# Kernel optimization log

Hardware: AMD Instinct MI355X
Metric: run time of the kernel (lower is better)

Reference implementation:

```python
import jax, jax.numpy as jnp
import numpy as np

# Dimensions
B, T_ENC, T_DEC = 64, 128, 64          # batch, encoder frames, max_video_length
DH, DV, CHUNK = 1024, 2048, 8          # dim_hidden, dim_video, ON-LSTM chunk size
NCH = DV // CHUNK                      # number of chunks (256)
G = 4 * DV + 2 * NCH                   # gate width of ON-LSTM cell


def setup_inputs() -> dict:
    key = jax.random.key(0)
    ks = jax.random.split(key, 6)
    s = lambda n: 1.0 / np.sqrt(n)
    return {
        "encoder_outputs": jax.random.normal(ks[0], (B, T_ENC, DH), jnp.float32),
        "encoder_hidden": jnp.zeros((1, B, DH), jnp.float32),  # unused by forward
        # Attention_update params: score over concat(enc_feat, query)
        "W_att1": (jax.random.normal(ks[1], (DH + DV, DH), jnp.float32) * s(DH + DV)),
        "b_att1": jnp.zeros((DH,), jnp.float32),
        "w_att2": (jax.random.normal(ks[2], (DH,), jnp.float32) * s(DH)),
        # ON-LSTM cell params (single layer: input DH -> hidden DV)
        "W_ih": (jax.random.normal(ks[3], (DH, G), jnp.float32) * s(DH)),
        "b_ih": jnp.zeros((G,), jnp.float32),
        "W_hh": (jax.random.normal(ks[4], (DV, G), jnp.float32) * s(DV)),
        "b_hh": jnp.zeros((G,), jnp.float32),
    }


def cumsoftmax(x):
    return jnp.cumsum(jax.nn.softmax(x, axis=-1), axis=-1)


def _decode(encoder_outputs, W_att1, b_att1, w_att2, W_ih, b_ih, W_hh, b_hh):
    b = encoder_outputs.shape[0]
    t_enc = encoder_outputs.shape[1]
    h0 = jnp.zeros((b, DV), encoder_outputs.dtype)
    c0 = jnp.zeros((b, NCH, CHUNK), encoder_outputs.dtype)

    def step(carry, _):
        h, c = carry
        # --- attention: additive score over encoder outputs, query = hidden ---
        q = jnp.broadcast_to(h[:, None, :], (b, t_enc, DV))
        feat = jnp.concatenate([encoder_outputs, q], axis=-1)        # (B,T,DH+DV)
        e = jnp.tanh(feat @ W_att1 + b_att1) @ w_att2                # (B,T)
        alpha = jax.nn.softmax(e, axis=-1)
        context = jnp.einsum("bt,btd->bd", alpha, encoder_outputs)  # (B,DH)
        # --- ON-LSTM cell ---
        gates = context @ W_ih + b_ih + h @ W_hh + b_hh              # (B,G)
        cingate = 1.0 - cumsoftmax(gates[:, :NCH])                   # master input gate
        cforgetgate = cumsoftmax(gates[:, NCH:2 * NCH])              # master forget gate
        r = gates[:, 2 * NCH:].reshape(b, 4 * NCH, CHUNK)
        o = jax.nn.sigmoid(r[:, :NCH])
        g = jnp.tanh(r[:, NCH:2 * NCH])
        i = jax.nn.sigmoid(r[:, 2 * NCH:3 * NCH])
        f = jax.nn.sigmoid(r[:, 3 * NCH:])
        cin = cingate[:, :, None]
        cfg = cforgetgate[:, :, None]
        overlap = cfg * cin
        fgate = f * overlap + (cfg - overlap)
        igate = i * overlap + (cin - overlap)
        cy = fgate * c + igate * g                                   # (B,NCH,CHUNK)
        hy = (o * jnp.tanh(cy)).reshape(b, DV)
        return (hy, cy), hy

    (_, _), outs = jax.lax.scan(step, (h0, c0), None, length=T_DEC)
    return jnp.transpose(outs, (1, 0, 2))  # (B, T_DEC, DV)


def reference(encoder_outputs, encoder_hidden, W_att1, b_att1, w_att2, W_ih, b_ih, W_hh, b_hh):
    return _decode(encoder_outputs, W_att1, b_att1, w_att2, W_ih, b_ih, W_hh, b_hh)
```

## Files before the change

kernel.cpp:

```cpp
#include <hip/hip_runtime.h>
#include <math.h>

#define BB   64
#define TENC 128
#define TDEC 64
#define DHH  1024
#define DVV  2048
#define NCHN 256
#define GG   8704
#define KTOT 3072

typedef unsigned short u16;
typedef __bf16 bf16x8 __attribute__((ext_vector_type(8)));
typedef float  f32x4  __attribute__((ext_vector_type(4)));

__device__ __forceinline__ float sigmoidf_(float x) { return 1.f / (1.f + expf(-x)); }
__device__ __forceinline__ u16 f2bf(float f) {
    unsigned u = __float_as_uint(f);
    unsigned r = (u + 0x7fffu + ((u >> 16) & 1u)) >> 16;
    return (u16)r;
}
__device__ __forceinline__ float bf2f(u16 s) { return __uint_as_float(((unsigned)s) << 16); }


__global__ __launch_bounds__(256) void k_P(const float* __restrict__ enc,
                                           const float* __restrict__ W1,
                                           const float* __restrict__ b1,
                                           float* __restrict__ P) {
    __shared__ float As[32][68];
    __shared__ float Bs[32][68];
    int j0 = blockIdx.x * 64;
    int m0 = blockIdx.y * 64;
    int tid = threadIdx.x;
    int jg = tid & 15, bg = tid >> 4;
    float acc[4][4] = {};
    for (int k0 = 0; k0 < DHH; k0 += 32) {
#pragma unroll
        for (int p = 0; p < 8; ++p) {
            int r = p * 8 + (tid >> 5);
            int kk = tid & 31;
            As[kk][r] = enc[(size_t)(m0 + r) * DHH + k0 + kk];
        }
#pragma unroll
        for (int p = 0; p < 8; ++p) {
            int kk = p * 4 + (tid >> 6);
            int jl = tid & 63;
            Bs[kk][jl] = W1[(size_t)(k0 + kk) * DHH + j0 + jl];
        }
        __syncthreads();
#pragma unroll
        for (int kk = 0; kk < 32; ++kk) {
            float4 a = *(const float4*)&As[kk][bg * 4];
            float4 b = *(const float4*)&Bs[kk][jg * 4];
            float av[4] = {a.x, a.y, a.z, a.w};
            float bv[4] = {b.x, b.y, b.z, b.w};
#pragma unroll
            for (int i = 0; i < 4; ++i)
#pragma unroll
                for (int j = 0; j < 4; ++j) acc[i][j] += av[i] * bv[j];
        }
        __syncthreads();
    }
    float4 bb = *(const float4*)&b1[j0 + jg * 4];
    float bia[4] = {bb.x, bb.y, bb.z, bb.w};
#pragma unroll
    for (int i = 0; i < 4; ++i) {
        int r = m0 + bg * 4 + i;
        float4 v = make_float4(acc[i][0] + bia[0], acc[i][1] + bia[1],
                               acc[i][2] + bia[2], acc[i][3] + bia[3]);
        *(float4*)&P[(size_t)r * DHH + j0 + jg * 4] = v;
    }
}

__global__ __launch_bounds__(256) void k_e(const float* __restrict__ P,
                                           const float* __restrict__ hWp,
                                           const float* __restrict__ w2,
                                           float* __restrict__ e) {
    int b = blockIdx.x, tg = blockIdx.y;
    __shared__ float hw[DHH];
    __shared__ float w2s[DHH];
    int tid = threadIdx.x;
#pragma unroll
    for (int p = 0; p < 4; ++p) {
        int d = p * 256 + tid;
        float s = 0.f;
#pragma unroll
        for (int ks = 0; ks < 8; ++ks) s += hWp[(ks * 64 + b) * DHH + d];
        hw[d] = s;
        w2s[d] = w2[d];
    }
    __syncthreads();
    int wave = tid >> 6, lane = tid & 63;
    const float* Pb = P + (size_t)b * TENC * DHH;
    for (int tt = 0; tt < 8; ++tt) {
        int t = tg * 32 + wave * 8 + tt;
        const float* Pr = Pb + (size_t)t * DHH;
        float s = 0.f;
#pragma unroll
        for (int i = 0; i < 16; ++i) {
            int d = i * 64 + lane;
            s += tanhf(Pr[d] + hw[d]) * w2s[d];
        }
#pragma unroll
        for (int off = 32; off > 0; off >>= 1) s += __shfl_down(s, off);
        if (lane == 0) e[b * TENC + t] = s;
    }
}


__global__ __launch_bounds__(256) void k_init2(float* __restrict__ c,
                                               u16* __restrict__ xh,
                                               u16* __restrict__ xl) {
    int i = blockIdx.x * 256 + threadIdx.x;
    xh[i] = 0; xl[i] = 0;
    if (i < BB * DVV) c[i] = 0.f;
}

template <bool LO>
__global__ __launch_bounds__(256) void k_cvt(const float* __restrict__ S1,
                                             const float* __restrict__ S2,
                                             int K1, int N, int K,
                                             u16* __restrict__ Dh,
                                             u16* __restrict__ Dl) {
    __shared__ float t[64][65];
    int n0 = blockIdx.x * 64, k0 = blockIdx.y * 64;
    int tid = threadIdx.x;
    int cn = tid & 63, r4 = tid >> 6;
#pragma unroll
    for (int p = 0; p < 16; ++p) {
        int kk = p * 4 + r4;
        int kg = k0 + kk;
        const float* src = (kg < K1) ? S1 + (size_t)kg * N : S2 + (size_t)(kg - K1) * N;
        t[kk][cn] = src[n0 + cn];
    }
    __syncthreads();
    int ck = tid & 63, n4 = tid >> 6;
#pragma unroll
    for (int p = 0; p < 16; ++p) {
        int nn = p * 4 + n4;
        float w = t[ck][nn];
        u16 hi = f2bf(w);
        size_t o = (size_t)(n0 + nn) * K + k0 + ck;
        Dh[o] = hi;
        if (LO) Dl[o] = f2bf(w - bf2f(hi));
    }
}

__global__ __launch_bounds__(256) void k_mma1(const u16* __restrict__ xh,
                                              const u16* __restrict__ Wta,
                                              float* __restrict__ hWp) {
    int n0 = blockIdx.x * 64;
    int kseg = blockIdx.y;
    int wv = threadIdx.x >> 6, l = threadIdx.x & 63;
    int lr = l & 15, lk = (l >> 4) * 8;
    int n = n0 + wv * 16 + lr;
    const u16* wp = Wta + (size_t)n * 2048 + lk;
    const u16* ap = xh + (size_t)lr * KTOT + 1024 + lk;
    f32x4 z = {0.f, 0.f, 0.f, 0.f};
    f32x4 acc[4];
#pragma unroll
    for (int mf = 0; mf < 4; ++mf) acc[mf] = z;
    int kend = kseg * 256 + 256;
    for (int k = kseg * 256; k < kend; k += 32) {
        bf16x8 bfrag = *(const bf16x8*)(wp + k);
#pragma unroll
        for (int mf = 0; mf < 4; ++mf) {
            bf16x8 a = *(const bf16x8*)(ap + (size_t)mf * 16 * KTOT + k);
            acc[mf] = __builtin_amdgcn_mfma_f32_16x16x32_bf16(a, bfrag, acc[mf], 0, 0, 0);
        }
    }
    float* dst = hWp + (size_t)kseg * 64 * DHH;
#pragma unroll
    for (int mf = 0; mf < 4; ++mf)
#pragma unroll
        for (int r = 0; r < 4; ++r) {
            int m = mf * 16 + (l >> 4) * 4 + r;
            dst[(size_t)m * DHH + n] = acc[mf][r];
        }
}

__global__ __launch_bounds__(256) void k_mma3(const u16* __restrict__ xh,
                                              const u16* __restrict__ xl,
                                              const u16* __restrict__ Wh,
                                              const u16* __restrict__ Wl,
                                              float* __restrict__ part) {
    int n0 = blockIdx.x * 64;
    int kseg = blockIdx.y;
    int wv = threadIdx.x >> 6, l = threadIdx.x & 63;
    int lr = l & 15, lk = (l >> 4) * 8;
    int n = n0 + wv * 16 + lr;
    const u16* wph = Wh + (size_t)n * KTOT + lk;
    const u16* wpl = Wl + (size_t)n * KTOT + lk;
    const u16* aph = xh + (size_t)lr * KTOT + lk;
    const u16* apl = xl + (size_t)lr * KTOT + lk;
    f32x4 z = {0.f, 0.f, 0.f, 0.f};
    f32x4 acc[4];
#pragma unroll
    for (int mf = 0; mf < 4; ++mf) acc[mf] = z;
    int kend = kseg * 1536 + 1536;
    for (int k = kseg * 1536; k < kend; k += 32) {
        bf16x8 bh = *(const bf16x8*)(wph + k);
        bf16x8 bl = *(const bf16x8*)(wpl + k);
#pragma unroll
        for (int mf = 0; mf < 4; ++mf) {
            size_t ao = (size_t)mf * 16 * KTOT + k;
            bf16x8 ah = *(const bf16x8*)(aph + ao);
            bf16x8 al = *(const bf16x8*)(apl + ao);
            acc[mf] = __builtin_amdgcn_mfma_f32_16x16x32_bf16(ah, bh, acc[mf], 0, 0, 0);
            acc[mf] = __builtin_amdgcn_mfma_f32_16x16x32_bf16(ah, bl, acc[mf], 0, 0, 0);
            acc[mf] = __builtin_amdgcn_mfma_f32_16x16x32_bf16(al, bh, acc[mf], 0, 0, 0);
        }
    }
    float* dst = part + (size_t)kseg * 64 * GG;
#pragma unroll
    for (int mf = 0; mf < 4; ++mf)
#pragma unroll
        for (int r = 0; r < 4; ++r) {
            int m = mf * 16 + (l >> 4) * 4 + r;
            dst[(size_t)m * GG + n] = acc[mf][r];
        }
}

__global__ __launch_bounds__(256) void k_sc2(const float* __restrict__ e,
                                             const float* __restrict__ enc,
                                             u16* __restrict__ xh,
                                             u16* __restrict__ xl) {
    int b = blockIdx.x, dg = blockIdx.y;
    __shared__ float al[TENC];
    __shared__ float red[256];
    int tid = threadIdx.x;
    float v = (tid < TENC) ? e[b * TENC + tid] : -3.0e38f;
    red[tid] = v;
    __syncthreads();
    for (int s = 128; s > 0; s >>= 1) {
        if (tid < s) red[tid] = fmaxf(red[tid], red[tid + s]);
        __syncthreads();
    }
    float mx = red[0];
    __syncthreads();
    float ex = (tid < TENC) ? expf(v - mx) : 0.f;
    red[tid] = ex;
    __syncthreads();
    for (int s = 128; s > 0; s >>= 1) {
        if (tid < s) red[tid] += red[tid + s];
        __syncthreads();
    }
    float inv = 1.f / red[0];
    if (tid < TENC) al[tid] = ex * inv;
    __syncthreads();
    int d = dg * 256 + tid;
    const float* ep = enc + (size_t)b * TENC * DHH + d;
    float acc = 0.f;
#pragma unroll 4
    for (int t = 0; t < TENC; ++t) acc += al[t] * ep[(size_t)t * DHH];
    u16 hi = f2bf(acc);
    xh[(size_t)b * KTOT + d] = hi;
    xl[(size_t)b * KTOT + d] = f2bf(acc - bf2f(hi));
}

__global__ __launch_bounds__(256) void k_pw2(const float* __restrict__ part,
                                             const float* __restrict__ bih,
                                             const float* __restrict__ bhh,
                                             u16* __restrict__ xh,
                                             u16* __restrict__ xl,
                                             float* __restrict__ c,
                                             float* __restrict__ out, int t) {
    int b = blockIdx.x;
    __shared__ float g[GG];
    __shared__ float cs1[NCHN], cs2[NCHN], t1[NCHN], t2[NCHN];
    int tid = threadIdx.x;
    for (int p = 0; p < 34; ++p) {
        int j = p * 256 + tid;
        float s = bih[j] + bhh[j] + part[(size_t)b * GG + j] + part[(size_t)(64 + b) * GG + j];
        g[j] = s;
    }
    __syncthreads();
    float x1 = g[tid], x2 = g[NCHN + tid];
    t1[tid] = x1; t2[tid] = x2;
    __syncthreads();
    for (int s = 128; s > 0; s >>= 1) {
        if (tid < s) { t1[tid] = fmaxf(t1[tid], t1[tid + s]); t2[tid] = fmaxf(t2[tid], t2[tid + s]); }
        __syncthreads();
    }
    float m1 = t1[0], m2 = t2[0];
    __syncthreads();
    float e1 = expf(x1 - m1), e2 = expf(x2 - m2);
    t1[tid] = e1; t2[tid] = e2;
    __syncthreads();
    for (int s = 128; s > 0; s >>= 1) {
        if (tid < s) { t1[tid] += t1[tid + s]; t2[tid] += t2[tid + s]; }
        __syncthreads();
    }
    float inv1 = 1.f / t1[0], inv2 = 1.f / t2[0];
    __syncthreads();
    cs1[tid] = e1; cs2[tid] = e2;
    __syncthreads();
    for (int off = 1; off < NCHN; off <<= 1) {
        float a1 = (tid >= off) ? cs1[tid - off] : 0.f;
        float a2 = (tid >= off) ? cs2[tid - off] : 0.f;
        __syncthreads();
        cs1[tid] += a1; cs2[tid] += a2;
        __syncthreads();
    }
    float* cb = c + (size_t)b * DVV;
    float* ob = out + ((size_t)b * TDEC + t) * DVV;
    u16* xhb = xh + (size_t)b * KTOT + 1024;
    u16* xlb = xl + (size_t)b * KTOT + 1024;
    for (int p = 0; p < 8; ++p) {
        int idx = p * 256 + tid;
        int ch = idx >> 3;
        float cin = 1.f - cs1[ch] * inv1;
        float cfg = cs2[ch] * inv2;
        float ov = cfg * cin;
        float oo = sigmoidf_(g[512 + idx]);
        float gg = tanhf(g[2560 + idx]);
        float ii = sigmoidf_(g[4608 + idx]);
        float ff = sigmoidf_(g[6656 + idx]);
        float fg = ff * ov + (cfg - ov);
        float ig = ii * ov + (cin - ov);
        float cy = fg * cb[idx] + ig * gg;
        cb[idx] = cy;
        float hy = oo * tanhf(cy);
        ob[idx] = hy;
        u16 hh = f2bf(hy);
        xhb[idx] = hh;
        xlb[idx] = f2bf(hy - bf2f(hh));
    }
}


__global__ __launch_bounds__(256) void k_init(float* __restrict__ h, float* __restrict__ c) {
    int i = blockIdx.x * 256 + threadIdx.x;
    h[i] = 0.f;
    c[i] = 0.f;
}

template <int KS>
__global__ __launch_bounds__(256) void k_skinny(const float* __restrict__ A1,
                                                const float* __restrict__ A2,
                                                const float* __restrict__ B1,
                                                const float* __restrict__ B2,
                                                int K1, int K2, int N,
                                                float* __restrict__ part) {
    __shared__ float As[32][68];
    __shared__ float Bs[32][68];
    int j0 = blockIdx.x * 64;
    int kseg = blockIdx.y;
    int tid = threadIdx.x;
    int jg = tid & 15, bg = tid >> 4;
    float acc[4][4] = {};
    for (int k0 = kseg * KS; k0 < (kseg + 1) * KS; k0 += 32) {
#pragma unroll
        for (int p = 0; p < 8; ++p) {
            int r = p * 8 + (tid >> 5);
            int kk = tid & 31;
            int k = k0 + kk;
            As[kk][r] = (k < K1) ? A1[r * K1 + k] : A2[r * K2 + (k - K1)];
        }
#pragma unroll
        for (int p = 0; p < 8; ++p) {
            int kk = p * 4 + (tid >> 6);
            int jl = tid & 63;
            int k = k0 + kk;
            Bs[kk][jl] = (k < K1) ? B1[(size_t)k * N + j0 + jl]
                                  : B2[(size_t)(k - K1) * N + j0 + jl];
        }
        __syncthreads();
#pragma unroll
        for (int kk = 0; kk < 32; ++kk) {
            float4 a = *(const float4*)&As[kk][bg * 4];
            float4 b = *(const float4*)&Bs[kk][jg * 4];
            float av[4] = {a.x, a.y, a.z, a.w};
            float bv[4] = {b.x, b.y, b.z, b.w};
#pragma unroll
            for (int i = 0; i < 4; ++i)
#pragma unroll
                for (int j = 0; j < 4; ++j) acc[i][j] += av[i] * bv[j];
        }
        __syncthreads();
    }
#pragma unroll
    for (int i = 0; i < 4; ++i) {
        int r = bg * 4 + i;
        float4 v = make_float4(acc[i][0], acc[i][1], acc[i][2], acc[i][3]);
        *(float4*)&part[(size_t)(kseg * 64 + r) * N + j0 + jg * 4] = v;
    }
}

__global__ __launch_bounds__(256) void k_sc_f32(const float* __restrict__ e,
                                                const float* __restrict__ enc,
                                                float* __restrict__ ctx) {
    int b = blockIdx.x, dg = blockIdx.y;
    __shared__ float al[TENC];
    __shared__ float red[256];
    int tid = threadIdx.x;
    float v = (tid < TENC) ? e[b * TENC + tid] : -3.0e38f;
    red[tid] = v;
    __syncthreads();
    for (int s = 128; s > 0; s >>= 1) {
        if (tid < s) red[tid] = fmaxf(red[tid], red[tid + s]);
        __syncthreads();
    }
    float mx = red[0];
    __syncthreads();
    float ex = (tid < TENC) ? expf(v - mx) : 0.f;
    red[tid] = ex;
    __syncthreads();
    for (int s = 128; s > 0; s >>= 1) {
        if (tid < s) red[tid] += red[tid + s];
        __syncthreads();
    }
    float inv = 1.f / red[0];
    if (tid < TENC) al[tid] = ex * inv;
    __syncthreads();
    int d = dg * 256 + tid;
    const float* ep = enc + (size_t)b * TENC * DHH + d;
    float acc = 0.f;
#pragma unroll 4
    for (int t = 0; t < TENC; ++t) acc += al[t] * ep[(size_t)t * DHH];
    ctx[b * DHH + d] = acc;
}

__global__ __launch_bounds__(256) void k_pw_f32(const float* __restrict__ part,
                                                const float* __restrict__ bih,
                                                const float* __restrict__ bhh,
                                                float* __restrict__ h,
                                                float* __restrict__ c,
                                                float* __restrict__ out, int t) {
    int b = blockIdx.x;
    __shared__ float g[GG];
    __shared__ float cs1[NCHN], cs2[NCHN], t1[NCHN], t2[NCHN];
    int tid = threadIdx.x;
    for (int p = 0; p < 34; ++p) {
        int j = p * 256 + tid;
        float s = bih[j] + bhh[j];
#pragma unroll
        for (int ks = 0; ks < 6; ++ks) s += part[(size_t)(ks * 64 + b) * GG + j];
        g[j] = s;
    }
    __syncthreads();
    float x1 = g[tid], x2 = g[NCHN + tid];
    t1[tid] = x1; t2[tid] = x2;
    __syncthreads();
    for (int s = 128; s > 0; s >>= 1) {
        if (tid < s) { t1[tid] = fmaxf(t1[tid], t1[tid + s]); t2[tid] = fmaxf(t2[tid], t2[tid + s]); }
        __syncthreads();
    }
    float m1 = t1[0], m2 = t2[0];
    __syncthreads();
    float e1 = expf(x1 - m1), e2 = expf(x2 - m2);
    t1[tid] = e1; t2[tid] = e2;
    __syncthreads();
    for (int s = 128; s > 0; s >>= 1) {
        if (tid < s) { t1[tid] += t1[tid + s]; t2[tid] += t2[tid + s]; }
        __syncthreads();
    }
    float inv1 = 1.f / t1[0], inv2 = 1.f / t2[0];
    __syncthreads();
    cs1[tid] = e1; cs2[tid] = e2;
    __syncthreads();
    for (int off = 1; off < NCHN; off <<= 1) {
        float a1 = (tid >= off) ? cs1[tid - off] : 0.f;
        float a2 = (tid >= off) ? cs2[tid - off] : 0.f;
        __syncthreads();
        cs1[tid] += a1; cs2[tid] += a2;
        __syncthreads();
    }
    float* cb = c + (size_t)b * DVV;
    float* hb = h + (size_t)b * DVV;
    float* ob = out + ((size_t)b * TDEC + t) * DVV;
    for (int p = 0; p < 8; ++p) {
        int idx = p * 256 + tid;
        int ch = idx >> 3;
        float cin = 1.f - cs1[ch] * inv1;
        float cfg = cs2[ch] * inv2;
        float ov = cfg * cin;
        float oo = sigmoidf_(g[512 + idx]);
        float gg = tanhf(g[2560 + idx]);
        float ii = sigmoidf_(g[4608 + idx]);
        float ff = sigmoidf_(g[6656 + idx]);
        float fg = ff * ov + (cfg - ov);
        float ig = ii * ov + (cin - ov);
        float cy = fg * cb[idx] + ig * gg;
        cb[idx] = cy;
        float hy = oo * tanhf(cy);
        hb[idx] = hy;
        ob[idx] = hy;
    }
}


extern "C" void kernel_launch(void* const* d_in, const int* in_sizes, int n_in,
                              void* d_out, int out_size, void* d_ws, size_t ws_size,
                              hipStream_t stream) {
    const float* enc    = (const float*)d_in[0];
    const float* W_att1 = (const float*)d_in[2];
    const float* b_att1 = (const float*)d_in[3];
    const float* w_att2 = (const float*)d_in[4];
    const float* W_ih   = (const float*)d_in[5];
    const float* b_ih   = (const float*)d_in[6];
    const float* W_hh   = (const float*)d_in[7];
    const float* b_hh   = (const float*)d_in[8];
    float* out = (float*)d_out;
    float* ws  = (float*)d_ws;

    if (ws_size >= 152600576ull) {
        float* P    = ws;
        float* hWp  = P + 8388608;
        float* ebuf = hWp + 524288;
        float* gp   = ebuf + 8192;
        float* c    = gp + 1114112;
        u16* xh  = (u16*)(c + 131072);
        u16* xl  = xh + 196608;
        u16* Wth = xl + 196608;
        u16* Wtl = Wth + 26738688;
        u16* Wta = Wtl + 26738688;

        k_init2<<<768, 256, 0, stream>>>(c, xh, xl);
        k_cvt<true><<<dim3(136, 48), 256, 0, stream>>>(W_ih, W_hh, 1024, GG, KTOT, Wth, Wtl);
        const float* Wh_att = W_att1 + 1024 * 1024;
        k_cvt<false><<<dim3(16, 32), 256, 0, stream>>>(Wh_att, Wh_att, 2048, DHH, 2048, Wta, Wta);
        k_P<<<dim3(16, 128), 256, 0, stream>>>(enc, W_att1, b_att1, P);

        for (int t = 0; t < TDEC; ++t) {
            k_mma1<<<dim3(16, 8), 256, 0, stream>>>(xh, Wta, hWp);
            k_e<<<dim3(BB, 4), 256, 0, stream>>>(P, hWp, w_att2, ebuf);
            k_sc2<<<dim3(BB, 4), 256, 0, stream>>>(ebuf, enc, xh, xl);
            k_mma3<<<dim3(136, 2), 256, 0, stream>>>(xh, xl, Wth, Wtl, gp);
            k_pw2<<<BB, 256, 0, stream>>>(gp, b_ih, b_hh, xh, xl, c, out, t);
        }
    } else if (ws_size >= 12591104ull * 4ull) {
        float* P    = ws;
        float* hWp  = P + 8388608;
        float* ebuf = hWp + 524288;
        float* ctx  = ebuf + 8192;
        float* gp   = ctx + 65536;
        float* h    = gp + 3342336;
        float* c    = h + 131072;

        k_init<<<512, 256, 0, stream>>>(h, c);
        k_P<<<dim3(16, 128), 256, 0, stream>>>(enc, W_att1, b_att1, P);

        const float* Wh_att = W_att1 + 1024 * 1024;
        for (int t = 0; t < TDEC; ++t) {
            k_skinny<256><<<dim3(16, 8), 256, 0, stream>>>(h, h, Wh_att, Wh_att,
                                                           2048, 2048, DHH, hWp);
            k_e<<<dim3(BB, 4), 256, 0, stream>>>(P, hWp, w_att2, ebuf);
            k_sc_f32<<<dim3(BB, 4), 256, 0, stream>>>(ebuf, enc, ctx);
            k_skinny<512><<<dim3(136, 6), 256, 0, stream>>>(ctx, h, W_ih, W_hh,
                                                            1024, 2048, GG, gp);
            k_pw_f32<<<BB, 256, 0, stream>>>(gp, b_ih, b_hh, h, c, out, t);
        }
    }
}
```

Measured before the change: 12.10 ms.

## Move precompute GEMM to split-bf16 MFMA, add in-block K-split and fast math

```diff
diff --git a/kernel.cpp b/kernel.cpp
--- a/kernel.cpp
+++ b/kernel.cpp
@@ -14,14 +14,110 @@
 typedef __bf16 bf16x8 __attribute__((ext_vector_type(8)));
 typedef float  f32x4  __attribute__((ext_vector_type(4)));
 
-__device__ __forceinline__ float sigmoidf_(float x) { return 1.f / (1.f + expf(-x)); }
 __device__ __forceinline__ u16 f2bf(float f) {
     unsigned u = __float_as_uint(f);
     unsigned r = (u + 0x7fffu + ((u >> 16) & 1u)) >> 16;
     return (u16)r;
 }
 __device__ __forceinline__ float bf2f(u16 s) { return __uint_as_float(((unsigned)s) << 16); }
-
+__device__ __forceinline__ float tanh_fast(float x) {
+    float xc = fminf(fmaxf(x, -15.f), 15.f);
+    float t = __expf(2.f * xc);
+    return 1.f - 2.f * __builtin_amdgcn_rcpf(t + 1.f);
+}
+__device__ __forceinline__ float sigmoid_fast(float x) {
+    float xc = fminf(fmaxf(x, -30.f), 30.f);
+    return __builtin_amdgcn_rcpf(1.f + __expf(-xc));
+}
+
+
+__global__ __launch_bounds__(256) void k_init2(float* __restrict__ c,
+                                               u16* __restrict__ xh,
+                                               u16* __restrict__ xl) {
+    int i = blockIdx.x * 256 + threadIdx.x;
+    xh[i] = 0; xl[i] = 0;
+    if (i < BB * DVV) c[i] = 0.f;
+}
+
+template <bool LO>
+__global__ __launch_bounds__(256) void k_cvt(const float* __restrict__ S1,
+                                             const float* __restrict__ S2,
+                                             int K1, int N, int K,
+                                             u16* __restrict__ Dh,
+                                             u16* __restrict__ Dl) {
+    __shared__ float t[64][65];
+    int n0 = blockIdx.x * 64, k0 = blockIdx.y * 64;
+    int tid = threadIdx.x;
+    int cn = tid & 63, r4 = tid >> 6;
+#pragma unroll
+    for (int p = 0; p < 16; ++p) {
+        int kk = p * 4 + r4;
+        int kg = k0 + kk;
+        const float* src = (kg < K1) ? S1 + (size_t)kg * N : S2 + (size_t)(kg - K1) * N;
+        t[kk][cn] = src[n0 + cn];
+    }
+    __syncthreads();
+    int ck = tid & 63, n4 = tid >> 6;
+#pragma unroll
+    for (int p = 0; p < 16; ++p) {
+        int nn = p * 4 + n4;
+        float w = t[ck][nn];
+        u16 hi = f2bf(w);
+        size_t o = (size_t)(n0 + nn) * K + k0 + ck;
+        Dh[o] = hi;
+        if (LO) Dl[o] = f2bf(w - bf2f(hi));
+    }
+}
+
+__global__ __launch_bounds__(256) void k_cvt_rm(const float* __restrict__ src,
+                                                u16* __restrict__ dh,
+                                                u16* __restrict__ dl, int n) {
+    for (int i = blockIdx.x * 256 + threadIdx.x; i < n; i += gridDim.x * 256) {
+        float w = src[i];
+        u16 hi = f2bf(w);
+        dh[i] = hi;
+        dl[i] = f2bf(w - bf2f(hi));
+    }
+}
+
+__global__ __launch_bounds__(256) void k_mmaP(const u16* __restrict__ ench,
+                                              const u16* __restrict__ encl,
+                                              const u16* __restrict__ W1h,
+                                              const u16* __restrict__ W1l,
+                                              const float* __restrict__ b1,
+                                              float* __restrict__ P) {
+    int n0 = blockIdx.x * 64, m0 = blockIdx.y * 64;
+    int wv = threadIdx.x >> 6, l = threadIdx.x & 63;
+    int lr = l & 15, lk = (l >> 4) * 8;
+    int n = n0 + wv * 16 + lr;
+    const u16* wph = W1h + (size_t)n * DHH + lk;
+    const u16* wpl = W1l + (size_t)n * DHH + lk;
+    const u16* aph = ench + (size_t)(m0 + lr) * DHH + lk;
+    const u16* apl = encl + (size_t)(m0 + lr) * DHH + lk;
+    f32x4 z = {0.f, 0.f, 0.f, 0.f};
+    f32x4 acc[4] = {z, z, z, z};
+    for (int k = 0; k < DHH; k += 32) {
+        bf16x8 bh = *(const bf16x8*)(wph + k);
+        bf16x8 bl = *(const bf16x8*)(wpl + k);
+#pragma unroll
+        for (int mf = 0; mf < 4; ++mf) {
+            size_t ao = (size_t)mf * 16 * DHH + k;
+            bf16x8 ah = *(const bf16x8*)(aph + ao);
+            bf16x8 al = *(const bf16x8*)(apl + ao);
+            acc[mf] = __builtin_amdgcn_mfma_f32_16x16x32_bf16(ah, bh, acc[mf], 0, 0, 0);
+            acc[mf] = __builtin_amdgcn_mfma_f32_16x16x32_bf16(ah, bl, acc[mf], 0, 0, 0);
+            acc[mf] = __builtin_amdgcn_mfma_f32_16x16x32_bf16(al, bh, acc[mf], 0, 0, 0);
+        }
+    }
+    float bias = b1[n];
+#pragma unroll
+    for (int mf = 0; mf < 4; ++mf)
+#pragma unroll
+        for (int r = 0; r < 4; ++r) {
+            int m = m0 + mf * 16 + (l >> 4) * 4 + r;
+            P[(size_t)m * DHH + n] = acc[mf][r] + bias;
+        }
+}
 
 __global__ __launch_bounds__(256) void k_P(const float* __restrict__ enc,
                                            const float* __restrict__ W1,
@@ -72,6 +168,109 @@
     }
 }
 
+
+__global__ __launch_bounds__(512) void k_mma1(const u16* __restrict__ xh,
+                                              const u16* __restrict__ Wta,
+                                              float* __restrict__ hWp) {
+    __shared__ float red[64 * 68];
+    int n0 = blockIdx.x * 64;
+    int kseg = blockIdx.y;
+    int tid = threadIdx.x;
+    int wv = tid >> 6, l = tid & 63;
+    int wn = wv & 3, kh = wv >> 2;
+    int lr = l & 15, lk = (l >> 4) * 8;
+    int n = n0 + wn * 16 + lr;
+    const u16* wp = Wta + (size_t)n * 2048 + lk;
+    const u16* ap = xh + (size_t)lr * KTOT + 1024 + lk;
+    f32x4 z = {0.f, 0.f, 0.f, 0.f};
+    f32x4 acc[4] = {z, z, z, z};
+    int kbeg = kseg * 256 + kh * 128;
+    for (int k = kbeg; k < kbeg + 128; k += 32) {
+        bf16x8 bfrag = *(const bf16x8*)(wp + k);
+#pragma unroll
+        for (int mf = 0; mf < 4; ++mf) {
+            bf16x8 a = *(const bf16x8*)(ap + (size_t)mf * 16 * KTOT + k);
+            acc[mf] = __builtin_amdgcn_mfma_f32_16x16x32_bf16(a, bfrag, acc[mf], 0, 0, 0);
+        }
+    }
+    int moff = (l >> 4) * 4;
+    if (kh == 0) {
+#pragma unroll
+        for (int mf = 0; mf < 4; ++mf)
+#pragma unroll
+            for (int r = 0; r < 4; ++r)
+                red[(mf * 16 + moff + r) * 68 + wn * 16 + lr] = acc[mf][r];
+    }
+    __syncthreads();
+    if (kh == 1) {
+        float* dst = hWp + (size_t)kseg * 64 * DHH;
+#pragma unroll
+        for (int mf = 0; mf < 4; ++mf)
+#pragma unroll
+            for (int r = 0; r < 4; ++r) {
+                int m = mf * 16 + moff + r;
+                dst[(size_t)m * DHH + n] = acc[mf][r] + red[m * 68 + wn * 16 + lr];
+            }
+    }
+}
+
+template <int SEG>
+__global__ __launch_bounds__(512) void k_mma3(const u16* __restrict__ xh,
+                                              const u16* __restrict__ xl,
+                                              const u16* __restrict__ Wh,
+                                              const u16* __restrict__ Wl,
+                                              float* __restrict__ part) {
+    __shared__ float red[64 * 68];
+    int n0 = blockIdx.x * 64;
+    int kseg = blockIdx.y;
+    int tid = threadIdx.x;
+    int wv = tid >> 6, l = tid & 63;
+    int wn = wv & 3, kh = wv >> 2;
+    int lr = l & 15, lk = (l >> 4) * 8;
+    int n = n0 + wn * 16 + lr;
+    const u16* wph = Wh + (size_t)n * KTOT + lk;
+    const u16* wpl = Wl + (size_t)n * KTOT + lk;
+    const u16* aph = xh + (size_t)lr * KTOT + lk;
+    const u16* apl = xl + (size_t)lr * KTOT + lk;
+    f32x4 z = {0.f, 0.f, 0.f, 0.f};
+    f32x4 acc[4] = {z, z, z, z};
+    const int KSEG = KTOT / SEG;
+    const int KH = KSEG / 2;
+    int kbeg = kseg * KSEG + kh * KH;
+    for (int k = kbeg; k < kbeg + KH; k += 32) {
+        bf16x8 bh = *(const bf16x8*)(wph + k);
+        bf16x8 bl = *(const bf16x8*)(wpl + k);
+#pragma unroll
+        for (int mf = 0; mf < 4; ++mf) {
+            size_t ao = (size_t)mf * 16 * KTOT + k;
+            bf16x8 ah = *(const bf16x8*)(aph + ao);
+            bf16x8 al = *(const bf16x8*)(apl + ao);
+            acc[mf] = __builtin_amdgcn_mfma_f32_16x16x32_bf16(ah, bh, acc[mf], 0, 0, 0);
+            acc[mf] = __builtin_amdgcn_mfma_f32_16x16x32_bf16(ah, bl, acc[mf], 0, 0, 0);
+            acc[mf] = __builtin_amdgcn_mfma_f32_16x16x32_bf16(al, bh, acc[mf], 0, 0, 0);
+        }
+    }
+    int moff = (l >> 4) * 4;
+    if (kh == 0) {
+#pragma unroll
+        for (int mf = 0; mf < 4; ++mf)
+#pragma unroll
+            for (int r = 0; r < 4; ++r)
+                red[(mf * 16 + moff + r) * 68 + wn * 16 + lr] = acc[mf][r];
+    }
+    __syncthreads();
+    if (kh == 1) {
+        float* dst = part + (size_t)kseg * 64 * GG;
+#pragma unroll
+        for (int mf = 0; mf < 4; ++mf)
+#pragma unroll
+            for (int r = 0; r < 4; ++r) {
+                int m = mf * 16 + moff + r;
+                dst[(size_t)m * GG + n] = acc[mf][r] + red[m * 68 + wn * 16 + lr];
+            }
+    }
+}
+
 __global__ __launch_bounds__(256) void k_e(const float* __restrict__ P,
                                            const float* __restrict__ hWp,
                                            const float* __restrict__ w2,
@@ -80,14 +279,15 @@
     __shared__ float hw[DHH];
     __shared__ float w2s[DHH];
     int tid = threadIdx.x;
-#pragma unroll
-    for (int p = 0; p < 4; ++p) {
-        int d = p * 256 + tid;
-        float s = 0.f;
-#pragma unroll
-        for (int ks = 0; ks < 8; ++ks) s += hWp[(ks * 64 + b) * DHH + d];
-        hw[d] = s;
-        w2s[d] = w2[d];
+    {
+        float4 s = {0.f, 0.f, 0.f, 0.f};
+#pragma unroll
+        for (int ks = 0; ks < 8; ++ks) {
+            float4 v = *(const float4*)&hWp[(size_t)(ks * 64 + b) * DHH + tid * 4];
+            s.x += v.x; s.y += v.y; s.z += v.z; s.w += v.w;
+        }
+        *(float4*)&hw[tid * 4] = s;
+        *(float4*)&w2s[tid * 4] = *(const float4*)&w2[tid * 4];
     }
     __syncthreads();
     int wave = tid >> 6, lane = tid & 63;
@@ -99,135 +299,22 @@
 #pragma unroll
         for (int i = 0; i < 16; ++i) {
             int d = i * 64 + lane;
-            s += tanhf(Pr[d] + hw[d]) * w2s[d];
+            s += tanh_fast(Pr[d] + hw[d]) * w2s[d];
         }
 #pragma unroll
         for (int off = 32; off > 0; off >>= 1) s += __shfl_down(s, off);
         if (lane == 0) e[b * TENC + t] = s;
     }
-}
-
-
-__global__ __launch_bounds__(256) void k_init2(float* __restrict__ c,
-                                               u16* __restrict__ xh,
-                                               u16* __restrict__ xl) {
-    int i = blockIdx.x * 256 + threadIdx.x;
-    xh[i] = 0; xl[i] = 0;
-    if (i < BB * DVV) c[i] = 0.f;
-}
-
-template <bool LO>
-__global__ __launch_bounds__(256) void k_cvt(const float* __restrict__ S1,
-                                             const float* __restrict__ S2,
-                                             int K1, int N, int K,
-                                             u16* __restrict__ Dh,
-                                             u16* __restrict__ Dl) {
-    __shared__ float t[64][65];
-    int n0 = blockIdx.x * 64, k0 = blockIdx.y * 64;
-    int tid = threadIdx.x;
-    int cn = tid & 63, r4 = tid >> 6;
-#pragma unroll
-    for (int p = 0; p < 16; ++p) {
-        int kk = p * 4 + r4;
-        int kg = k0 + kk;
-        const float* src = (kg < K1) ? S1 + (size_t)kg * N : S2 + (size_t)(kg - K1) * N;
-        t[kk][cn] = src[n0 + cn];
-    }
-    __syncthreads();
-    int ck = tid & 63, n4 = tid >> 6;
-#pragma unroll
-    for (int p = 0; p < 16; ++p) {
-        int nn = p * 4 + n4;
-        float w = t[ck][nn];
-        u16 hi = f2bf(w);
-        size_t o = (size_t)(n0 + nn) * K + k0 + ck;
-        Dh[o] = hi;
-        if (LO) Dl[o] = f2bf(w - bf2f(hi));
-    }
-}
-
-__global__ __launch_bounds__(256) void k_mma1(const u16* __restrict__ xh,
-                                              const u16* __restrict__ Wta,
-                                              float* __restrict__ hWp) {
-    int n0 = blockIdx.x * 64;
-    int kseg = blockIdx.y;
-    int wv = threadIdx.x >> 6, l = threadIdx.x & 63;
-    int lr = l & 15, lk = (l >> 4) * 8;
-    int n = n0 + wv * 16 + lr;
-    const u16* wp = Wta + (size_t)n * 2048 + lk;
-    const u16* ap = xh + (size_t)lr * KTOT + 1024 + lk;
-    f32x4 z = {0.f, 0.f, 0.f, 0.f};
-    f32x4 acc[4];
-#pragma unroll
-    for (int mf = 0; mf < 4; ++mf) acc[mf] = z;
-    int kend = kseg * 256 + 256;
-    for (int k = kseg * 256; k < kend; k += 32) {
-        bf16x8 bfrag = *(const bf16x8*)(wp + k);
-#pragma unroll
-        for (int mf = 0; mf < 4; ++mf) {
-            bf16x8 a = *(const bf16x8*)(ap + (size_t)mf * 16 * KTOT + k);
-            acc[mf] = __builtin_amdgcn_mfma_f32_16x16x32_bf16(a, bfrag, acc[mf], 0, 0, 0);
-        }
-    }
-    float* dst = hWp + (size_t)kseg * 64 * DHH;
-#pragma unroll
-    for (int mf = 0; mf < 4; ++mf)
-#pragma unroll
-        for (int r = 0; r < 4; ++r) {
-            int m = mf * 16 + (l >> 4) * 4 + r;
-            dst[(size_t)m * DHH + n] = acc[mf][r];
-        }
-}
-
-__global__ __launch_bounds__(256) void k_mma3(const u16* __restrict__ xh,
-                                              const u16* __restrict__ xl,
-                                              const u16* __restrict__ Wh,
-                                              const u16* __restrict__ Wl,
-                                              float* __restrict__ part) {
-    int n0 = blockIdx.x * 64;
-    int kseg = blockIdx.y;
-    int wv = threadIdx.x >> 6, l = threadIdx.x & 63;
-    int lr = l & 15, lk = (l >> 4) * 8;
-    int n = n0 + wv * 16 + lr;
-    const u16* wph = Wh + (size_t)n * KTOT + lk;
-    const u16* wpl = Wl + (size_t)n * KTOT + lk;
-    const u16* aph = xh + (size_t)lr * KTOT + lk;
-    const u16* apl = xl + (size_t)lr * KTOT + lk;
-    f32x4 z = {0.f, 0.f, 0.f, 0.f};
-    f32x4 acc[4];
-#pragma unroll
-    for (int mf = 0; mf < 4; ++mf) acc[mf] = z;
-    int kend = kseg * 1536 + 1536;
-    for (int k = kseg * 1536; k < kend; k += 32) {
-        bf16x8 bh = *(const bf16x8*)(wph + k);
-        bf16x8 bl = *(const bf16x8*)(wpl + k);
-#pragma unroll
-        for (int mf = 0; mf < 4; ++mf) {
-            size_t ao = (size_t)mf * 16 * KTOT + k;
-            bf16x8 ah = *(const bf16x8*)(aph + ao);
-            bf16x8 al = *(const bf16x8*)(apl + ao);
-            acc[mf] = __builtin_amdgcn_mfma_f32_16x16x32_bf16(ah, bh, acc[mf], 0, 0, 0);
-            acc[mf] = __builtin_amdgcn_mfma_f32_16x16x32_bf16(ah, bl, acc[mf], 0, 0, 0);
-            acc[mf] = __builtin_amdgcn_mfma_f32_16x16x32_bf16(al, bh, acc[mf], 0, 0, 0);
-        }
-    }
-    float* dst = part + (size_t)kseg * 64 * GG;
-#pragma unroll
-    for (int mf = 0; mf < 4; ++mf)
-#pragma unroll
-        for (int r = 0; r < 4; ++r) {
-            int m = mf * 16 + (l >> 4) * 4 + r;
-            dst[(size_t)m * GG + n] = acc[mf][r];
-        }
 }
 
 __global__ __launch_bounds__(256) void k_sc2(const float* __restrict__ e,
                                              const float* __restrict__ enc,
                                              u16* __restrict__ xh,
                                              u16* __restrict__ xl) {
-    int b = blockIdx.x, dg = blockIdx.y;
+    int b = blockIdx.x, dq = blockIdx.y;
     __shared__ float al[TENC];
     __shared__ float red[256];
+    __shared__ float4 pr[4][64];
     int tid = threadIdx.x;
     float v = (tid < TENC) ? e[b * TENC + tid] : -3.0e38f;
     red[tid] = v;
@@ -238,7 +325,7 @@
     }
     float mx = red[0];
     __syncthreads();
-    float ex = (tid < TENC) ? expf(v - mx) : 0.f;
+    float ex = (tid < TENC) ? __expf(v - mx) : 0.f;
     red[tid] = ex;
     __syncthreads();
     for (int s = 128; s > 0; s >>= 1) {
@@ -248,17 +335,35 @@
     float inv = 1.f / red[0];
     if (tid < TENC) al[tid] = ex * inv;
     __syncthreads();
-    int d = dg * 256 + tid;
-    const float* ep = enc + (size_t)b * TENC * DHH + d;
-    float acc = 0.f;
-#pragma unroll 4
-    for (int t = 0; t < TENC; ++t) acc += al[t] * ep[(size_t)t * DHH];
-    u16 hi = f2bf(acc);
-    xh[(size_t)b * KTOT + d] = hi;
-    xl[(size_t)b * KTOT + d] = f2bf(acc - bf2f(hi));
-}
-
-__global__ __launch_bounds__(256) void k_pw2(const float* __restrict__ part,
+    int w = tid >> 6, l = tid & 63;
+    int dbase = dq * 256 + l * 4;
+    const float* ep = enc + ((size_t)b * TENC + w * 32) * DHH + dbase;
+    float4 acc = {0.f, 0.f, 0.f, 0.f};
+#pragma unroll 8
+    for (int tt = 0; tt < 32; ++tt) {
+        float a = al[w * 32 + tt];
+        float4 vv = *(const float4*)(ep + (size_t)tt * DHH);
+        acc.x += a * vv.x; acc.y += a * vv.y; acc.z += a * vv.z; acc.w += a * vv.w;
+    }
+    pr[w][l] = acc;
+    __syncthreads();
+    if (tid < 64) {
+        float4 a0 = pr[0][tid], a1 = pr[1][tid], a2 = pr[2][tid], a3 = pr[3][tid];
+        float r0 = a0.x + a1.x + a2.x + a3.x;
+        float r1 = a0.y + a1.y + a2.y + a3.y;
+        float r2 = a0.z + a1.z + a2.z + a3.z;
+        float r3 = a0.w + a1.w + a2.w + a3.w;
+        size_t o = (size_t)b * KTOT + dq * 256 + tid * 4;
+        u16 h0 = f2bf(r0), h1 = f2bf(r1), h2 = f2bf(r2), h3 = f2bf(r3);
+        ushort4 hv = {h0, h1, h2, h3};
+        ushort4 lv = {f2bf(r0 - bf2f(h0)), f2bf(r1 - bf2f(h1)),
+                      f2bf(r2 - bf2f(h2)), f2bf(r3 - bf2f(h3))};
+        *(ushort4*)&xh[o] = hv;
+        *(ushort4*)&xl[o] = lv;
+    }
+}
+
+__global__ __launch_bounds__(256) void k_pw2(const float* __restrict__ part, int nseg,
                                              const float* __restrict__ bih,
                                              const float* __restrict__ bhh,
                                              u16* __restrict__ xh,
@@ -271,7 +376,8 @@
     int tid = threadIdx.x;
     for (int p = 0; p < 34; ++p) {
         int j = p * 256 + tid;
-        float s = bih[j] + bhh[j] + part[(size_t)b * GG + j] + part[(size_t)(64 + b) * GG + j];
+        float s = bih[j] + bhh[j];
+        for (int ks = 0; ks < nseg; ++ks) s += part[(size_t)(ks * 64 + b) * GG + j];
         g[j] = s;
     }
     __syncthreads();
@@ -284,7 +390,7 @@
     }
     float m1 = t1[0], m2 = t2[0];
     __syncthreads();
-    float e1 = expf(x1 - m1), e2 = expf(x2 - m2);
+    float e1 = __expf(x1 - m1), e2 = __expf(x2 - m2);
     t1[tid] = e1; t2[tid] = e2;
     __syncthreads();
     for (int s = 128; s > 0; s >>= 1) {
@@ -312,180 +418,19 @@
         float cin = 1.f - cs1[ch] * inv1;
         float cfg = cs2[ch] * inv2;
         float ov = cfg * cin;
-        float oo = sigmoidf_(g[512 + idx]);
-        float gg = tanhf(g[2560 + idx]);
-        float ii = sigmoidf_(g[4608 + idx]);
-        float ff = sigmoidf_(g[6656 + idx]);
+        float oo = sigmoid_fast(g[512 + idx]);
+        float gg = tanh_fast(g[2560 + idx]);
+        float ii = sigmoid_fast(g[4608 + idx]);
+        float ff = sigmoid_fast(g[6656 + idx]);
         float fg = ff * ov + (cfg - ov);
         float ig = ii * ov + (cin - ov);
         float cy = fg * cb[idx] + ig * gg;
         cb[idx] = cy;
-        float hy = oo * tanhf(cy);
+        float hy = oo * tanh_fast(cy);
         ob[idx] = hy;
         u16 hh = f2bf(hy);
         xhb[idx] = hh;
         xlb[idx] = f2bf(hy - bf2f(hh));
-    }
-}
-
-
-__global__ __launch_bounds__(256) void k_init(float* __restrict__ h, float* __restrict__ c) {
-    int i = blockIdx.x * 256 + threadIdx.x;
-    h[i] = 0.f;
-    c[i] = 0.f;
-}
-
-template <int KS>
-__global__ __launch_bounds__(256) void k_skinny(const float* __restrict__ A1,
-                                                const float* __restrict__ A2,
-                                                const float* __restrict__ B1,
-                                                const float* __restrict__ B2,
-                                                int K1, int K2, int N,
-                                                float* __restrict__ part) {
-    __shared__ float As[32][68];
-    __shared__ float Bs[32][68];
-    int j0 = blockIdx.x * 64;
-    int kseg = blockIdx.y;
-    int tid = threadIdx.x;
-    int jg = tid & 15, bg = tid >> 4;
-    float acc[4][4] = {};
-    for (int k0 = kseg * KS; k0 < (kseg + 1) * KS; k0 += 32) {
-#pragma unroll
-        for (int p = 0; p < 8; ++p) {
-            int r = p * 8 + (tid >> 5);
-            int kk = tid & 31;
-            int k = k0 + kk;
-            As[kk][r] = (k < K1) ? A1[r * K1 + k] : A2[r * K2 + (k - K1)];
-        }
-#pragma unroll
-        for (int p = 0; p < 8; ++p) {
-            int kk = p * 4 + (tid >> 6);
-            int jl = tid & 63;
-            int k = k0 + kk;
-            Bs[kk][jl] = (k < K1) ? B1[(size_t)k * N + j0 + jl]
-                                  : B2[(size_t)(k - K1) * N + j0 + jl];
-        }
-        __syncthreads();
-#pragma unroll
-        for (int kk = 0; kk < 32; ++kk) {
-            float4 a = *(const float4*)&As[kk][bg * 4];
-            float4 b = *(const float4*)&Bs[kk][jg * 4];
-            float av[4] = {a.x, a.y, a.z, a.w};
-            float bv[4] = {b.x, b.y, b.z, b.w};
-#pragma unroll
-            for (int i = 0; i < 4; ++i)
-#pragma unroll
-                for (int j = 0; j < 4; ++j) acc[i][j] += av[i] * bv[j];
-        }
-        __syncthreads();
-    }
-#pragma unroll
-    for (int i = 0; i < 4; ++i) {
-        int r = bg * 4 + i;
-        float4 v = make_float4(acc[i][0], acc[i][1], acc[i][2], acc[i][3]);
-        *(float4*)&part[(size_t)(kseg * 64 + r) * N + j0 + jg * 4] = v;
-    }
-}
-
-__global__ __launch_bounds__(256) void k_sc_f32(const float* __restrict__ e,
-                                                const float* __restrict__ enc,
-                                                float* __restrict__ ctx) {
-    int b = blockIdx.x, dg = blockIdx.y;
-    __shared__ float al[TENC];
-    __shared__ float red[256];
-    int tid = threadIdx.x;
-    float v = (tid < TENC) ? e[b * TENC + tid] : -3.0e38f;
-    red[tid] = v;
-    __syncthreads();
-    for (int s = 128; s > 0; s >>= 1) {
-        if (tid < s) red[tid] = fmaxf(red[tid], red[tid + s]);
-        __syncthreads();
-    }
-    float mx = red[0];
-    __syncthreads();
-    float ex = (tid < TENC) ? expf(v - mx) : 0.f;
-    red[tid] = ex;
-    __syncthreads();
-    for (int s = 128; s > 0; s >>= 1) {
-        if (tid < s) red[tid] += red[tid + s];
-        __syncthreads();
-    }
-    float inv = 1.f / red[0];
-    if (tid < TENC) al[tid] = ex * inv;
-    __syncthreads();
-    int d = dg * 256 + tid;
-    const float* ep = enc + (size_t)b * TENC * DHH + d;
-    float acc = 0.f;
-#pragma unroll 4
-    for (int t = 0; t < TENC; ++t) acc += al[t] * ep[(size_t)t * DHH];
-    ctx[b * DHH + d] = acc;
-}
-
-__global__ __launch_bounds__(256) void k_pw_f32(const float* __restrict__ part,
-                                                const float* __restrict__ bih,
-                                                const float* __restrict__ bhh,
-                                                float* __restrict__ h,
-                                                float* __restrict__ c,
-                                                float* __restrict__ out, int t) {
-    int b = blockIdx.x;
-    __shared__ float g[GG];
-    __shared__ float cs1[NCHN], cs2[NCHN], t1[NCHN], t2[NCHN];
-    int tid = threadIdx.x;
-    for (int p = 0; p < 34; ++p) {
-        int j = p * 256 + tid;
-        float s = bih[j] + bhh[j];
-#pragma unroll
-        for (int ks = 0; ks < 6; ++ks) s += part[(size_t)(ks * 64 + b) * GG + j];
-        g[j] = s;
-    }
-    __syncthreads();
-    float x1 = g[tid], x2 = g[NCHN + tid];
-    t1[tid] = x1; t2[tid] = x2;
-    __syncthreads();
-    for (int s = 128; s > 0; s >>= 1) {
-        if (tid < s) { t1[tid] = fmaxf(t1[tid], t1[tid + s]); t2[tid] = fmaxf(t2[tid], t2[tid + s]); }
-        __syncthreads();
-    }
-    float m1 = t1[0], m2 = t2[0];
-    __syncthreads();
-    float e1 = expf(x1 - m1), e2 = expf(x2 - m2);
-    t1[tid] = e1; t2[tid] = e2;
-    __syncthreads();
-    for (int s = 128; s > 0; s >>= 1) {
-        if (tid < s) { t1[tid] += t1[tid + s]; t2[tid] += t2[tid + s]; }
-        __syncthreads();
-    }
-    float inv1 = 1.f / t1[0], inv2 = 1.f / t2[0];
-    __syncthreads();
-    cs1[tid] = e1; cs2[tid] = e2;
-    __syncthreads();
-    for (int off = 1; off < NCHN; off <<= 1) {
-        float a1 = (tid >= off) ? cs1[tid - off] : 0.f;
-        float a2 = (tid >= off) ? cs2[tid - off] : 0.f;
-        __syncthreads();
-        cs1[tid] += a1; cs2[tid] += a2;
-        __syncthreads();
-    }
-    float* cb = c + (size_t)b * DVV;
-    float* hb = h + (size_t)b * DVV;
-    float* ob = out + ((size_t)b * TDEC + t) * DVV;
-    for (int p = 0; p < 8; ++p) {
-        int idx = p * 256 + tid;
-        int ch = idx >> 3;
-        float cin = 1.f - cs1[ch] * inv1;
-        float cfg = cs2[ch] * inv2;
-        float ov = cfg * cin;
-        float oo = sigmoidf_(g[512 + idx]);
-        float gg = tanhf(g[2560 + idx]);
-        float ii = sigmoidf_(g[4608 + idx]);
-        float ff = sigmoidf_(g[6656 + idx]);
-        float fg = ff * ov + (cfg - ov);
-        float ig = ii * ov + (cin - ov);
-        float cy = fg * cb[idx] + ig * gg;
-        cb[idx] = cy;
-        float hy = oo * tanhf(cy);
-        hb[idx] = hy;
-        ob[idx] = hy;
     }
 }
 
@@ -503,8 +448,40 @@
     const float* b_hh   = (const float*)d_in[8];
     float* out = (float*)d_out;
     float* ws  = (float*)d_ws;
-
-    if (ws_size >= 152600576ull) {
+    const float* Wh_att = W_att1 + 1024 * 1024;
+
+    if (ws_size >= 182976512ull) {
+        float* P   = ws;
+        float* c   = P + 8388608;
+        u16* Wth   = (u16*)(c + 131072);
+        u16* Wtl   = Wth + 26738688;
+        u16* Wta   = Wtl + 26738688;
+        u16* region = Wta + 2097152;
+        u16* ench = region;
+        u16* encl = ench + 8388608;
+        u16* W1h  = encl + 8388608;
+        u16* W1l  = W1h + 1048576;
+        float* gp   = (float*)region;
+        float* hWp  = gp + 2228224;
+        float* ebuf = hWp + 524288;
+        u16* xh     = (u16*)(ebuf + 8192);
+        u16* xl     = xh + 196608;
+
+        k_cvt<true><<<dim3(136, 48), 256, 0, stream>>>(W_ih, W_hh, 1024, GG, KTOT, Wth, Wtl);
+        k_cvt<false><<<dim3(16, 32), 256, 0, stream>>>(Wh_att, Wh_att, 2048, DHH, 2048, Wta, Wta);
+        k_cvt<true><<<dim3(16, 16), 256, 0, stream>>>(W_att1, W_att1, 2048, DHH, DHH, W1h, W1l);
+        k_cvt_rm<<<4096, 256, 0, stream>>>(enc, ench, encl, 8388608);
+        k_mmaP<<<dim3(16, 128), 256, 0, stream>>>(ench, encl, W1h, W1l, b_att1, P);
+        k_init2<<<768, 256, 0, stream>>>(c, xh, xl);
+
+        for (int t = 0; t < TDEC; ++t) {
+            k_mma1<<<dim3(16, 8), 512, 0, stream>>>(xh, Wta, hWp);
+            k_e<<<dim3(BB, 4), 256, 0, stream>>>(P, hWp, w_att2, ebuf);
+            k_sc2<<<dim3(BB, 4), 256, 0, stream>>>(ebuf, enc, xh, xl);
+            k_mma3<4><<<dim3(136, 4), 512, 0, stream>>>(xh, xl, Wth, Wtl, gp);
+            k_pw2<<<BB, 256, 0, stream>>>(gp, 4, b_ih, b_hh, xh, xl, c, out, t);
+        }
+    } else if (ws_size >= 152600576ull) {
         float* P    = ws;
         float* hWp  = P + 8388608;
         float* ebuf = hWp + 524288;
@@ -516,40 +493,17 @@
         u16* Wtl = Wth + 26738688;
         u16* Wta = Wtl + 26738688;
 
-        k_init2<<<768, 256, 0, stream>>>(c, xh, xl);
         k_cvt<true><<<dim3(136, 48), 256, 0, stream>>>(W_ih, W_hh, 1024, GG, KTOT, Wth, Wtl);
-        const float* Wh_att = W_att1 + 1024 * 1024;
         k_cvt<false><<<dim3(16, 32), 256, 0, stream>>>(Wh_att, Wh_att, 2048, DHH, 2048, Wta, Wta);
         k_P<<<dim3(16, 128), 256, 0, stream>>>(enc, W_att1, b_att1, P);
+        k_init2<<<768, 256, 0, stream>>>(c, xh, xl);
 
         for (int t = 0; t < TDEC; ++t) {
-            k_mma1<<<dim3(16, 8), 256, 0, stream>>>(xh, Wta, hWp);
+            k_mma1<<<dim3(16, 8), 512, 0, stream>>>(xh, Wta, hWp);
             k_e<<<dim3(BB, 4), 256, 0, stream>>>(P, hWp, w_att2, ebuf);
             k_sc2<<<dim3(BB, 4), 256, 0, stream>>>(ebuf, enc, xh, xl);
-            k_mma3<<<dim3(136, 2), 256, 0, stream>>>(xh, xl, Wth, Wtl, gp);
-            k_pw2<<<BB, 256, 0, stream>>>(gp, b_ih, b_hh, xh, xl, c, out, t);
-        }
-    } else if (ws_size >= 12591104ull * 4ull) {
-        float* P    = ws;
-        float* hWp  = P + 8388608;
-        float* ebuf = hWp + 524288;
-        float* ctx  = ebuf + 8192;
-        float* gp   = ctx + 65536;
-        float* h    = gp + 3342336;
-        float* c    = h + 131072;
-
-        k_init<<<512, 256, 0, stream>>>(h, c);
-        k_P<<<dim3(16, 128), 256, 0, stream>>>(enc, W_att1, b_att1, P);
-
-        const float* Wh_att = W_att1 + 1024 * 1024;
-        for (int t = 0; t < TDEC; ++t) {
-            k_skinny<256><<<dim3(16, 8), 256, 0, stream>>>(h, h, Wh_att, Wh_att,
-                                                           2048, 2048, DHH, hWp);
-            k_e<<<dim3(BB, 4), 256, 0, stream>>>(P, hWp, w_att2, ebuf);
-            k_sc_f32<<<dim3(BB, 4), 256, 0, stream>>>(ebuf, enc, ctx);
-            k_skinny<512><<<dim3(136, 6), 256, 0, stream>>>(ctx, h, W_ih, W_hh,
-                                                            1024, 2048, GG, gp);
-            k_pw_f32<<<BB, 256, 0, stream>>>(gp, b_ih, b_hh, h, c, out, t);
-        }
-    }
-}
+            k_mma3<2><<<dim3(136, 2), 512, 0, stream>>>(xh, xl, Wth, Wtl, gp);
+            k_pw2<<<BB, 256, 0, stream>>>(gp, 2, b_ih, b_hh, xh, xl, c, out, t);
+        }
+    }
+}
```

After: 10.14 ms. 16.2% less time.
